# Kernel tuning notes

Measured on AMD Instinct MI355X. Metric: run time of the kernel, lower is better.

## Reference

```python
import jax, jax.numpy as jnp
import numpy as np

VOCAB, TAGS, EDIM, HDIM = 128, 8, 256, 1024
B, T = 1024, 128


def setup_inputs() -> dict:
    key = jax.random.key(0)
    ks = jax.random.split(key, 8)
    s = 0.02
    graph_ids = jax.random.randint(ks[0], (B, T), 0, VOCAB)
    emb = jax.random.normal(ks[1], (VOCAB, EDIM), jnp.float32) * s
    emb = emb.at[0].set(0.0)  # padding_idx=0
    W_ih = jax.random.normal(ks[2], (HDIM, EDIM), jnp.float32) * s
    W_hh = jax.random.normal(ks[3], (HDIM, HDIM), jnp.float32) * s
    b_ih = jax.random.normal(ks[4], (HDIM,), jnp.float32) * s
    b_hh = jax.random.normal(ks[5], (HDIM,), jnp.float32) * s
    W_out = jax.random.normal(ks[6], (TAGS, HDIM), jnp.float32) * s
    b_out = jax.random.normal(ks[7], (TAGS,), jnp.float32) * s
    return {"graph_ids": graph_ids, "emb": emb, "W_ih": W_ih, "W_hh": W_hh,
            "b_ih": b_ih, "b_hh": b_hh, "W_out": W_out, "b_out": b_out}


def reference(graph_ids, emb, W_ih, W_hh, b_ih, b_hh, W_out, b_out):
    batch, max_len = graph_ids.shape
    x = emb[graph_ids]                               # [B, T, E]
    mask = (graph_ids != 0).astype(jnp.float32)      # [B, T]
    seq_lengths = mask.sum(axis=1)                   # [B]
    h0 = jnp.zeros((batch, W_hh.shape[0]), x.dtype)

    def step(h, inp):
        x_t, t = inp                                  # x_t: [B, E]
        nh = jnp.tanh(x_t @ W_ih.T + b_ih + h @ W_hh.T + b_hh)
        m = (t < seq_lengths).astype(h.dtype)[:, None]
        h = m * nh + (1.0 - m) * h
        return h, h @ W_out.T + b_out                 # emit tag logits [B, TAGS]

    xs = (jnp.swapaxes(x, 0, 1), jnp.arange(max_len))
    _, ys = jax.lax.scan(step, h0, xs)               # ys: [T, B, TAGS]
    return jnp.swapaxes(ys, 0, 1)                    # [B, T, TAGS]
```

## Files before the change

### kernel.cpp

```cpp
#include <hip/hip_runtime.h>
#include <hip/hip_bf16.h>

typedef __bf16 bf16;
typedef __bf16 bf16x8 __attribute__((ext_vector_type(8)));
typedef float  f32x4  __attribute__((ext_vector_type(4)));

#define TT    128
#define BB    1024
#define VOCAB 128
#define EE    256
#define HH    1024
#define NTAGS 8
#define PW    1032

#define OFF_SW 0
#define OFF_ST (OFF_SW + 64 * PW * 2)
#define OFF_WO (OFF_ST + 64 * 72 * 2)
#define OFF_ID (OFF_WO + NTAGS * 64 * 4)
#define OFF_SL (OFF_ID + 256)
#define LDS_TOTAL (OFF_SL + 256)

#define BARSTRIDE 128

__global__ __launch_bounds__(256) void cvt_k(const float* __restrict__ s,
                                             bf16* __restrict__ d, int n) {
    int i = (blockIdx.x * 256 + threadIdx.x) * 4;
    if (i >= n) return;
    float4 v = *(const float4*)(s + i);
    bf16 o[4] = {(bf16)v.x, (bf16)v.y, (bf16)v.z, (bf16)v.w};
    *(short4*)(d + i) = *(short4*)o;
}

__global__ __launch_bounds__(256) void seqlen_k(const int* __restrict__ ids,
                                                int* __restrict__ sl,
                                                int* __restrict__ idsT) {
    int b = blockIdx.x * 256 + threadIdx.x;
    int c = 0;
    for (int t = 0; t < TT; ++t) {
        int v = ids[b * TT + t];
        idsT[t * BB + b] = v;
        c += (v != 0) ? 1 : 0;
    }
    sl[b] = c;
}

__global__ __launch_bounds__(256) void xp_k(const float* __restrict__ emb,
                                            const float* __restrict__ W_ih,
                                            const float* __restrict__ b_ih,
                                            const float* __restrict__ b_hh,
                                            float* __restrict__ XP) {
    __shared__ float se[EE];
    const int v = blockIdx.x;
    se[threadIdx.x] = emb[v * EE + threadIdx.x];
    __syncthreads();
    const int c0 = threadIdx.x * 4;
    float s0 = 0.f, s1 = 0.f, s2 = 0.f, s3 = 0.f;
    for (int e = 0; e < EE; e += 4) {
        float4 ev = *(const float4*)(se + e);
        float4 w0 = *(const float4*)(W_ih + (c0 + 0) * EE + e);
        float4 w1 = *(const float4*)(W_ih + (c0 + 1) * EE + e);
        float4 w2 = *(const float4*)(W_ih + (c0 + 2) * EE + e);
        float4 w3 = *(const float4*)(W_ih + (c0 + 3) * EE + e);
        s0 += ev.x * w0.x + ev.y * w0.y + ev.z * w0.z + ev.w * w0.w;
        s1 += ev.x * w1.x + ev.y * w1.y + ev.z * w1.z + ev.w * w1.w;
        s2 += ev.x * w2.x + ev.y * w2.y + ev.z * w2.z + ev.w * w2.w;
        s3 += ev.x * w3.x + ev.y * w3.y + ev.z * w3.z + ev.w * w3.w;
    }
    XP[v * HH + c0 + 0] = s0 + b_ih[c0 + 0] + b_hh[c0 + 0];
    XP[v * HH + c0 + 1] = s1 + b_ih[c0 + 1] + b_hh[c0 + 1];
    XP[v * HH + c0 + 2] = s2 + b_ih[c0 + 2] + b_hh[c0 + 2];
    XP[v * HH + c0 + 3] = s3 + b_ih[c0 + 3] + b_hh[c0 + 3];
}

__global__ __launch_bounds__(256)
void rnn_persist(const int*   __restrict__ idsT,
                 const float* __restrict__ XP,
                 const bf16*  __restrict__ Whh,
                 const float* __restrict__ W_out,
                 const int*   __restrict__ sl,
                 bf16* h0, bf16* h1,
                 float* __restrict__ y_part,
                 unsigned* __restrict__ bar)
{
    extern __shared__ __align__(16) char smem[];
    bf16*  sW   = (bf16*)(smem + OFF_SW);
    bf16*  sT   = (bf16*)(smem + OFF_ST);
    float* sWo  = (float*)(smem + OFF_WO);
    int*   sIds = (int*)(smem + OFF_ID);
    int*   sSl  = (int*)(smem + OFF_SL);

    const int tid = threadIdx.x;
    const int xcd = blockIdx.x & 7;
    const int w   = blockIdx.x >> 3;
    const int gm  = xcd * 2 + (w >> 4);
    const int gn  = w & 15;
    const int Mbase = gm * 64, Nbase = gn * 64;

    for (int i = tid; i < 64 * 128; i += 256) {
        int n = i >> 7, g = i & 127;
        *(int4*)(sW + n * PW + g * 8) =
            *(const int4*)(Whh + (size_t)(Nbase + n) * HH + g * 8);
    }
    if (tid < 128) {
        int tg = tid >> 4, c = (tid & 15) * 4;
        *(float4*)(sWo + tg * 64 + c) = *(const float4*)(W_out + tg * HH + Nbase + c);
    }
    if (tid < 64) sSl[tid] = sl[Mbase + tid];
    __syncthreads();

    const int wave = tid >> 6, lane = tid & 63;
    const int quad = lane >> 4, l15 = lane & 15;
    const int wm = (wave >> 1) * 32, wn = (wave & 1) * 32;
    const bf16* pB0 = sW + (wn + l15) * PW;
    const bf16* pB1 = sW + (wn + 16 + l15) * PW;

    unsigned tgt = 0;
    for (int s = 0; s < TT; ++s) {
        const bf16* hp = (s & 1) ? h1 : h0;
        bf16*       hn = (s & 1) ? h0 : h1;

        if (tid < 64) sIds[tid] = idsT[s * BB + Mbase + tid];

        f32x4 acc[2][2];
#pragma unroll
        for (int a = 0; a < 2; ++a)
#pragma unroll
            for (int b = 0; b < 2; ++b) {
                f32x4 z = {0.f, 0.f, 0.f, 0.f};
                acc[a][b] = z;
            }

        const bf16* pa0 = hp + (size_t)(Mbase + wm + l15) * HH + quad * 8;
        const bf16* pa1 = pa0 + (size_t)16 * HH;
        int4 ca0[4], ca1[4];
#pragma unroll
        for (int u = 0; u < 4; ++u) {
            ca0[u] = *(const int4*)(pa0 + u * 32);
            ca1[u] = *(const int4*)(pa1 + u * 32);
        }
#pragma unroll
        for (int jj = 0; jj < 32; jj += 4) {
            int4 na0[4], na1[4];
            if (jj < 28) {
#pragma unroll
                for (int u = 0; u < 4; ++u) {
                    na0[u] = *(const int4*)(pa0 + (jj + 4 + u) * 32);
                    na1[u] = *(const int4*)(pa1 + (jj + 4 + u) * 32);
                }
            }
#pragma unroll
            for (int u = 0; u < 4; ++u) {
                const int j = jj + u;
                bf16x8 b0 = *(const bf16x8*)(pB0 + j * 32 + quad * 8);
                bf16x8 b1 = *(const bf16x8*)(pB1 + j * 32 + quad * 8);
                bf16x8 a0 = __builtin_bit_cast(bf16x8, ca0[u]);
                bf16x8 a1 = __builtin_bit_cast(bf16x8, ca1[u]);
                acc[0][0] = __builtin_amdgcn_mfma_f32_16x16x32_bf16(a0, b0, acc[0][0], 0, 0, 0);
                acc[0][1] = __builtin_amdgcn_mfma_f32_16x16x32_bf16(a0, b1, acc[0][1], 0, 0, 0);
                acc[1][0] = __builtin_amdgcn_mfma_f32_16x16x32_bf16(a1, b0, acc[1][0], 0, 0, 0);
                acc[1][1] = __builtin_amdgcn_mfma_f32_16x16x32_bf16(a1, b1, acc[1][1], 0, 0, 0);
            }
            if (jj < 28) {
#pragma unroll
                for (int u = 0; u < 4; ++u) { ca0[u] = na0[u]; ca1[u] = na1[u]; }
            }
        }

        float xv[2][2][4];
#pragma unroll
        for (int sm = 0; sm < 2; ++sm)
#pragma unroll
            for (int sn = 0; sn < 2; ++sn)
#pragma unroll
                for (int rr = 0; rr < 4; ++rr) {
                    int row = wm + sm * 16 + quad * 4 + rr;
                    int col = wn + sn * 16 + l15;
                    xv[sm][sn][rr] = XP[(size_t)sIds[row] * HH + Nbase + col];
                }
#pragma unroll
        for (int sm = 0; sm < 2; ++sm)
#pragma unroll
            for (int sn = 0; sn < 2; ++sn)
#pragma unroll
                for (int rr = 0; rr < 4; ++rr) {
                    int row = wm + sm * 16 + quad * 4 + rr;
                    int col = wn + sn * 16 + l15;
                    float pre = acc[sm][sn][rr] + xv[sm][sn][rr];
                    pre = fminf(15.f, fmaxf(-15.f, pre));
                    float e = __expf(2.f * pre);
                    float nh = (e - 1.f) / (e + 1.f);
                    bf16 hv;
                    if (s < sSl[row]) hv = (bf16)nh;
                    else hv = hp[(size_t)(Mbase + row) * HH + Nbase + col];
                    sT[row * 72 + col] = hv;
                }
        __syncthreads();

        {
            const int r = tid >> 2, q = tid & 3;
            const bf16* srcp = sT + r * 72 + q * 16;
            int4 w0 = *(const int4*)(srcp);
            int4 w1 = *(const int4*)(srcp + 8);
            unsigned long long u0 = ((unsigned long long)(unsigned)w0.y << 32) | (unsigned)w0.x;
            unsigned long long u1 = ((unsigned long long)(unsigned)w0.w << 32) | (unsigned)w0.z;
            unsigned long long u2 = ((unsigned long long)(unsigned)w1.y << 32) | (unsigned)w1.x;
            unsigned long long u3 = ((unsigned long long)(unsigned)w1.w << 32) | (unsigned)w1.z;
            unsigned long long* hd =
                (unsigned long long*)(hn + (size_t)(Mbase + r) * HH + Nbase + q * 16);
            __hip_atomic_store(hd + 0, u0, __ATOMIC_RELAXED, __HIP_MEMORY_SCOPE_AGENT);
            __hip_atomic_store(hd + 1, u1, __ATOMIC_RELAXED, __HIP_MEMORY_SCOPE_AGENT);
            __hip_atomic_store(hd + 2, u2, __ATOMIC_RELAXED, __HIP_MEMORY_SCOPE_AGENT);
            __hip_atomic_store(hd + 3, u3, __ATOMIC_RELAXED, __HIP_MEMORY_SCOPE_AGENT);

            bf16x8 hv0 = __builtin_bit_cast(bf16x8, w0);
            bf16x8 hv1 = __builtin_bit_cast(bf16x8, w1);
            float lg[NTAGS];
#pragma unroll
            for (int tg = 0; tg < NTAGS; ++tg) {
                const float* ww = sWo + tg * 64 + q * 16;
                float p = 0.f;
#pragma unroll
                for (int j = 0; j < 8; ++j) p += (float)hv0[j] * ww[j];
#pragma unroll
                for (int j = 0; j < 8; ++j) p += (float)hv1[j] * ww[8 + j];
                p += __shfl_xor(p, 1);
                p += __shfl_xor(p, 2);
                lg[tg] = p;
            }
            float* yb = y_part + ((size_t)gn * BB + Mbase + r) * (TT * NTAGS)
                      + s * NTAGS + 2 * q;
            yb[0] = lg[2 * q];
            yb[1] = lg[2 * q + 1];
        }

        __syncthreads();
        tgt += 16;
        if (tid == 0) {
            __hip_atomic_fetch_add(&bar[gm * BARSTRIDE], 1u, __ATOMIC_RELAXED,
                                   __HIP_MEMORY_SCOPE_AGENT);
            while (__hip_atomic_load(&bar[gm * BARSTRIDE], __ATOMIC_RELAXED,
                                     __HIP_MEMORY_SCOPE_AGENT) < tgt)
                __builtin_amdgcn_s_sleep(1);
            __builtin_amdgcn_fence(__ATOMIC_ACQUIRE, "agent");
        }
        __syncthreads();
    }
}

__global__ __launch_bounds__(256) void reduce_bias_k(const float* __restrict__ yp,
                                                     const float* __restrict__ b_out,
                                                     float* __restrict__ out) {
    int idx = blockIdx.x * 256 + threadIdx.x;
    float4 s0 = *(const float4*)(b_out);
    float4 s1 = *(const float4*)(b_out + 4);
#pragma unroll
    for (int gn = 0; gn < 16; ++gn) {
        const float* p = yp + (size_t)gn * BB * TT * NTAGS + (size_t)idx * NTAGS;
        float4 a = *(const float4*)(p);
        float4 b = *(const float4*)(p + 4);
        s0.x += a.x; s0.y += a.y; s0.z += a.z; s0.w += a.w;
        s1.x += b.x; s1.y += b.y; s1.z += b.z; s1.w += b.w;
    }
    *(float4*)(out + (size_t)idx * NTAGS)     = s0;
    *(float4*)(out + (size_t)idx * NTAGS + 4) = s1;
}

extern "C" void kernel_launch(void* const* d_in, const int* in_sizes, int n_in,
                              void* d_out, int out_size, void* d_ws, size_t ws_size,
                              hipStream_t stream) {
    const int*   ids   = (const int*)d_in[0];
    const float* emb   = (const float*)d_in[1];
    const float* W_ih  = (const float*)d_in[2];
    const float* W_hh  = (const float*)d_in[3];
    const float* b_ih  = (const float*)d_in[4];
    const float* b_hh  = (const float*)d_in[5];
    const float* W_out = (const float*)d_in[6];
    const float* b_out = (const float*)d_in[7];
    float* out = (float*)d_out;

    char* ws = (char*)d_ws;
    size_t off = 0;
    int*      sl     = (int*)(ws + off);      off += 4096;
    int*      idsT   = (int*)(ws + off);      off += (size_t)BB * TT * 4;
    float*    XP     = (float*)(ws + off);    off += (size_t)VOCAB * HH * 4;
    bf16*     Whh16  = (bf16*)(ws + off);     off += (size_t)HH * HH * 2;
    bf16*     h0     = (bf16*)(ws + off);     off += (size_t)BB * HH * 2;
    bf16*     h1     = (bf16*)(ws + off);     off += (size_t)BB * HH * 2;
    float*    y_part = (float*)(ws + off);    off += (size_t)16 * BB * TT * NTAGS * 4;
    unsigned* bar    = (unsigned*)(ws + off); off += 16 * BARSTRIDE * 4;
    if (ws_size < off) return;

    (void)hipMemsetAsync(bar, 0, 16 * BARSTRIDE * 4, stream);
    (void)hipMemsetAsync(h0, 0, (size_t)BB * HH * 2, stream);

    cvt_k<<<(HH * HH / 4 + 255) / 256, 256, 0, stream>>>(W_hh, Whh16, HH * HH);
    xp_k<<<VOCAB, 256, 0, stream>>>(emb, W_ih, b_ih, b_hh, XP);
    seqlen_k<<<4, 256, 0, stream>>>(ids, sl, idsT);

    (void)hipFuncSetAttribute((const void*)rnn_persist,
                              hipFuncAttributeMaxDynamicSharedMemorySize, LDS_TOTAL);
    {
        const int*   a0 = idsT; const float* a1 = XP;  const bf16* a2 = Whh16;
        const float* a3 = W_out; const int*  a4 = sl;
        bf16* a5 = h0; bf16* a6 = h1; float* a7 = y_part; unsigned* a8 = bar;
        void* args[] = {&a0, &a1, &a2, &a3, &a4, &a5, &a6, &a7, &a8};
        (void)hipLaunchCooperativeKernel((const void*)rnn_persist, dim3(256), dim3(256),
                                         args, LDS_TOTAL, stream);
    }

    reduce_bias_k<<<BB * TT / 256, 256, 0, stream>>>(y_part, b_out, out);
}
```

Baseline: 1.803 ms.

## Double wave count per block with 16-row MFMA tiles and full A-prefetch

```diff
diff --git a/kernel.cpp b/kernel.cpp
--- a/kernel.cpp
+++ b/kernel.cpp
@@ -11,7 +11,7 @@
 #define EE    256
 #define HH    1024
 #define NTAGS 8
-#define PW    1032
+#define PW    1034
 
 #define OFF_SW 0
 #define OFF_ST (OFF_SW + 64 * PW * 2)
@@ -72,7 +72,7 @@
     XP[v * HH + c0 + 3] = s3 + b_ih[c0 + 3] + b_hh[c0 + 3];
 }
 
-__global__ __launch_bounds__(256)
+__global__ __launch_bounds__(512, 2)
 void rnn_persist(const int*   __restrict__ idsT,
                  const float* __restrict__ XP,
                  const bf16*  __restrict__ Whh,
@@ -96,7 +96,7 @@
     const int gn  = w & 15;
     const int Mbase = gm * 64, Nbase = gn * 64;
 
-    for (int i = tid; i < 64 * 128; i += 256) {
+    for (int i = tid; i < 64 * 128; i += 512) {
         int n = i >> 7, g = i & 127;
         *(int4*)(sW + n * PW + g * 8) =
             *(const int4*)(Whh + (size_t)(Nbase + n) * HH + g * 8);
@@ -110,7 +110,8 @@
 
     const int wave = tid >> 6, lane = tid & 63;
     const int quad = lane >> 4, l15 = lane & 15;
-    const int wm = (wave >> 1) * 32, wn = (wave & 1) * 32;
+    const int wm16 = (wave >> 1) * 16;
+    const int wn   = (wave & 1) * 32;
     const bf16* pB0 = sW + (wn + l15) * PW;
     const bf16* pB1 = sW + (wn + 16 + l15) * PW;
 
@@ -121,116 +122,73 @@
 
         if (tid < 64) sIds[tid] = idsT[s * BB + Mbase + tid];
 
-        f32x4 acc[2][2];
-#pragma unroll
-        for (int a = 0; a < 2; ++a)
-#pragma unroll
-            for (int b = 0; b < 2; ++b) {
-                f32x4 z = {0.f, 0.f, 0.f, 0.f};
-                acc[a][b] = z;
+        const bf16* pa = hp + (size_t)(Mbase + wm16 + l15) * HH + quad * 8;
+        int4 ca[32];
+#pragma unroll
+        for (int u = 0; u < 32; ++u) ca[u] = *(const int4*)(pa + u * 32);
+
+        f32x4 acc0 = {0.f, 0.f, 0.f, 0.f};
+        f32x4 acc1 = {0.f, 0.f, 0.f, 0.f};
+
+#pragma unroll
+        for (int j = 0; j < 32; ++j) {
+            bf16x8 b0 = *(const bf16x8*)(pB0 + j * 32 + quad * 8);
+            bf16x8 b1 = *(const bf16x8*)(pB1 + j * 32 + quad * 8);
+            bf16x8 a  = __builtin_bit_cast(bf16x8, ca[j]);
+            acc0 = __builtin_amdgcn_mfma_f32_16x16x32_bf16(a, b0, acc0, 0, 0, 0);
+            acc1 = __builtin_amdgcn_mfma_f32_16x16x32_bf16(a, b1, acc1, 0, 0, 0);
+        }
+
+        float xv[2][4], hpv[2][4];
+#pragma unroll
+        for (int sn = 0; sn < 2; ++sn)
+#pragma unroll
+            for (int rr = 0; rr < 4; ++rr) {
+                int row = wm16 + quad * 4 + rr;
+                int col = wn + sn * 16 + l15;
+                xv[sn][rr]  = XP[(size_t)sIds[row] * HH + Nbase + col];
+                hpv[sn][rr] = (float)hp[(size_t)(Mbase + row) * HH + Nbase + col];
             }
-
-        const bf16* pa0 = hp + (size_t)(Mbase + wm + l15) * HH + quad * 8;
-        const bf16* pa1 = pa0 + (size_t)16 * HH;
-        int4 ca0[4], ca1[4];
-#pragma unroll
-        for (int u = 0; u < 4; ++u) {
-            ca0[u] = *(const int4*)(pa0 + u * 32);
-            ca1[u] = *(const int4*)(pa1 + u * 32);
-        }
-#pragma unroll
-        for (int jj = 0; jj < 32; jj += 4) {
-            int4 na0[4], na1[4];
-            if (jj < 28) {
-#pragma unroll
-                for (int u = 0; u < 4; ++u) {
-                    na0[u] = *(const int4*)(pa0 + (jj + 4 + u) * 32);
-                    na1[u] = *(const int4*)(pa1 + (jj + 4 + u) * 32);
-                }
+        const f32x4* accp[2] = {&acc0, &acc1};
+#pragma unroll
+        for (int sn = 0; sn < 2; ++sn)
+#pragma unroll
+            for (int rr = 0; rr < 4; ++rr) {
+                int row = wm16 + quad * 4 + rr;
+                int col = wn + sn * 16 + l15;
+                float pre = (*accp[sn])[rr] + xv[sn][rr];
+                pre = fminf(15.f, fmaxf(-15.f, pre));
+                float e = __expf(2.f * pre);
+                float nh = (e - 1.f) / (e + 1.f);
+                sT[row * 72 + col] = (s < sSl[row]) ? (bf16)nh : (bf16)hpv[sn][rr];
             }
-#pragma unroll
-            for (int u = 0; u < 4; ++u) {
-                const int j = jj + u;
-                bf16x8 b0 = *(const bf16x8*)(pB0 + j * 32 + quad * 8);
-                bf16x8 b1 = *(const bf16x8*)(pB1 + j * 32 + quad * 8);
-                bf16x8 a0 = __builtin_bit_cast(bf16x8, ca0[u]);
-                bf16x8 a1 = __builtin_bit_cast(bf16x8, ca1[u]);
-                acc[0][0] = __builtin_amdgcn_mfma_f32_16x16x32_bf16(a0, b0, acc[0][0], 0, 0, 0);
-                acc[0][1] = __builtin_amdgcn_mfma_f32_16x16x32_bf16(a0, b1, acc[0][1], 0, 0, 0);
-                acc[1][0] = __builtin_amdgcn_mfma_f32_16x16x32_bf16(a1, b0, acc[1][0], 0, 0, 0);
-                acc[1][1] = __builtin_amdgcn_mfma_f32_16x16x32_bf16(a1, b1, acc[1][1], 0, 0, 0);
-            }
-            if (jj < 28) {
-#pragma unroll
-                for (int u = 0; u < 4; ++u) { ca0[u] = na0[u]; ca1[u] = na1[u]; }
-            }
-        }
-
-        float xv[2][2][4];
-#pragma unroll
-        for (int sm = 0; sm < 2; ++sm)
-#pragma unroll
-            for (int sn = 0; sn < 2; ++sn)
-#pragma unroll
-                for (int rr = 0; rr < 4; ++rr) {
-                    int row = wm + sm * 16 + quad * 4 + rr;
-                    int col = wn + sn * 16 + l15;
-                    xv[sm][sn][rr] = XP[(size_t)sIds[row] * HH + Nbase + col];
-                }
-#pragma unroll
-        for (int sm = 0; sm < 2; ++sm)
-#pragma unroll
-            for (int sn = 0; sn < 2; ++sn)
-#pragma unroll
-                for (int rr = 0; rr < 4; ++rr) {
-                    int row = wm + sm * 16 + quad * 4 + rr;
-                    int col = wn + sn * 16 + l15;
-                    float pre = acc[sm][sn][rr] + xv[sm][sn][rr];
-                    pre = fminf(15.f, fmaxf(-15.f, pre));
-                    float e = __expf(2.f * pre);
-                    float nh = (e - 1.f) / (e + 1.f);
-                    bf16 hv;
-                    if (s < sSl[row]) hv = (bf16)nh;
-                    else hv = hp[(size_t)(Mbase + row) * HH + Nbase + col];
-                    sT[row * 72 + col] = hv;
-                }
         __syncthreads();
 
         {
-            const int r = tid >> 2, q = tid & 3;
-            const bf16* srcp = sT + r * 72 + q * 16;
-            int4 w0 = *(const int4*)(srcp);
-            int4 w1 = *(const int4*)(srcp + 8);
-            unsigned long long u0 = ((unsigned long long)(unsigned)w0.y << 32) | (unsigned)w0.x;
-            unsigned long long u1 = ((unsigned long long)(unsigned)w0.w << 32) | (unsigned)w0.z;
-            unsigned long long u2 = ((unsigned long long)(unsigned)w1.y << 32) | (unsigned)w1.x;
-            unsigned long long u3 = ((unsigned long long)(unsigned)w1.w << 32) | (unsigned)w1.z;
+            const int r = tid >> 3, q8 = tid & 7;
+            const bf16* srcp = sT + r * 72 + q8 * 8;
+            int4 wv = *(const int4*)(srcp);
+            unsigned long long u0 = ((unsigned long long)(unsigned)wv.y << 32) | (unsigned)wv.x;
+            unsigned long long u1 = ((unsigned long long)(unsigned)wv.w << 32) | (unsigned)wv.z;
             unsigned long long* hd =
-                (unsigned long long*)(hn + (size_t)(Mbase + r) * HH + Nbase + q * 16);
+                (unsigned long long*)(hn + (size_t)(Mbase + r) * HH + Nbase + q8 * 8);
             __hip_atomic_store(hd + 0, u0, __ATOMIC_RELAXED, __HIP_MEMORY_SCOPE_AGENT);
             __hip_atomic_store(hd + 1, u1, __ATOMIC_RELAXED, __HIP_MEMORY_SCOPE_AGENT);
-            __hip_atomic_store(hd + 2, u2, __ATOMIC_RELAXED, __HIP_MEMORY_SCOPE_AGENT);
-            __hip_atomic_store(hd + 3, u3, __ATOMIC_RELAXED, __HIP_MEMORY_SCOPE_AGENT);
-
-            bf16x8 hv0 = __builtin_bit_cast(bf16x8, w0);
-            bf16x8 hv1 = __builtin_bit_cast(bf16x8, w1);
-            float lg[NTAGS];
+
+            bf16x8 hv = __builtin_bit_cast(bf16x8, wv);
+            float mytag = 0.f;
 #pragma unroll
             for (int tg = 0; tg < NTAGS; ++tg) {
-                const float* ww = sWo + tg * 64 + q * 16;
+                const float* ww = sWo + tg * 64 + q8 * 8;
                 float p = 0.f;
 #pragma unroll
-                for (int j = 0; j < 8; ++j) p += (float)hv0[j] * ww[j];
-#pragma unroll
-                for (int j = 0; j < 8; ++j) p += (float)hv1[j] * ww[8 + j];
+                for (int j = 0; j < 8; ++j) p += (float)hv[j] * ww[j];
                 p += __shfl_xor(p, 1);
                 p += __shfl_xor(p, 2);
-                lg[tg] = p;
+                p += __shfl_xor(p, 4);
+                if (q8 == tg) mytag = p;
             }
-            float* yb = y_part + ((size_t)gn * BB + Mbase + r) * (TT * NTAGS)
-                      + s * NTAGS + 2 * q;
-            yb[0] = lg[2 * q];
-            yb[1] = lg[2 * q + 1];
+            y_part[(((size_t)gn * TT + s) * BB + Mbase + r) * NTAGS + q8] = mytag;
         }
 
         __syncthreads();
@@ -251,18 +209,20 @@
                                                      const float* __restrict__ b_out,
                                                      float* __restrict__ out) {
     int idx = blockIdx.x * 256 + threadIdx.x;
+    int t = idx >> 10, b = idx & 1023;
     float4 s0 = *(const float4*)(b_out);
     float4 s1 = *(const float4*)(b_out + 4);
 #pragma unroll
     for (int gn = 0; gn < 16; ++gn) {
-        const float* p = yp + (size_t)gn * BB * TT * NTAGS + (size_t)idx * NTAGS;
+        const float* p = yp + (((size_t)gn * TT + t) * BB + b) * NTAGS;
         float4 a = *(const float4*)(p);
-        float4 b = *(const float4*)(p + 4);
+        float4 c = *(const float4*)(p + 4);
         s0.x += a.x; s0.y += a.y; s0.z += a.z; s0.w += a.w;
-        s1.x += b.x; s1.y += b.y; s1.z += b.z; s1.w += b.w;
-    }
-    *(float4*)(out + (size_t)idx * NTAGS)     = s0;
-    *(float4*)(out + (size_t)idx * NTAGS + 4) = s1;
+        s1.x += c.x; s1.y += c.y; s1.z += c.z; s1.w += c.w;
+    }
+    float* o = out + ((size_t)b * TT + t) * NTAGS;
+    *(float4*)(o)     = s0;
+    *(float4*)(o + 4) = s1;
 }
 
 extern "C" void kernel_launch(void* const* d_in, const int* in_sizes, int n_in,
@@ -304,7 +264,7 @@
         const float* a3 = W_out; const int*  a4 = sl;
         bf16* a5 = h0; bf16* a6 = h1; float* a7 = y_part; unsigned* a8 = bar;
         void* args[] = {&a0, &a1, &a2, &a3, &a4, &a5, &a6, &a7, &a8};
-        (void)hipLaunchCooperativeKernel((const void*)rnn_persist, dim3(256), dim3(256),
+        (void)hipLaunchCooperativeKernel((const void*)rnn_persist, dim3(256), dim3(512),
                                          args, LDS_TOTAL, stream);
     }
 
```

Result: slower. 2.526 ms (+40.1%).
